# Kernel tuning notes

Measured on AMD Instinct MI355X. Metric: run time of the kernel, lower is better.

The kernel has to match this reference:

```python
import jax, jax.numpy as jnp
import numpy as np

N_NODES = 50000
IN_DIM = 256
EDGE_DIM = 128
OUT_DIM = 128
EDGE_OUT_DIM = 128
N_EDGES = 1600000
NEG_SLOPE = 0.01


def leaky_relu(x):
    return jnp.where(x >= 0, x, NEG_SLOPE * x)


def _kaiming(key, out_d, in_d):
    # kaiming_uniform with a=0.01, leaky_relu gain
    gain = np.sqrt(2.0 / (1.0 + 0.01 ** 2))
    bound = gain * np.sqrt(3.0 / in_d)
    return jax.random.uniform(key, (out_d, in_d), jnp.float32, -bound, bound)


def setup_inputs() -> dict:
    key = jax.random.key(0)
    ks = jax.random.split(key, 9)
    x = jax.random.normal(ks[0], (N_NODES, IN_DIM), jnp.float32)
    edge_index = jax.random.randint(ks[1], (2, N_EDGES), 0, N_NODES, jnp.int64)
    edge_attr = jax.random.normal(ks[2], (N_EDGES, EDGE_DIM), jnp.float32)
    W_e = _kaiming(ks[3], OUT_DIM, EDGE_DIM)
    W_hu = _kaiming(ks[4], OUT_DIM, IN_DIM)
    W_hw = _kaiming(ks[5], OUT_DIM, IN_DIM)
    W2 = _kaiming(ks[6], OUT_DIM, IN_DIM)
    W_emb = _kaiming(ks[7], OUT_DIM, IN_DIM)
    W_attr = _kaiming(ks[8], EDGE_OUT_DIM, OUT_DIM)
    return {"x": x, "edge_index": edge_index, "edge_attr": edge_attr,
            "W_e": W_e, "W_hu": W_hu, "W_hw": W_hw,
            "W2": W2, "W_emb": W_emb, "W_attr": W_attr}


def reference(x, edge_index, edge_attr, W_e, W_hu, W_hw, W2, W_emb, W_attr):
    src, tgt = edge_index[0], edge_index[1]
    # project node features once (N x d), then gather per edge -> avoids E-sized GEMMs
    hu = x @ W_hu.T   # [N, out]
    hw = x @ W_hw.T   # [N, out]
    messages = leaky_relu(edge_attr @ W_e.T + hu[src] + hw[tgt])  # [E, out]
    # scatter_mean over target nodes
    sums = jax.ops.segment_sum(messages, tgt, num_segments=N_NODES)
    counts = jax.ops.segment_sum(jnp.ones((messages.shape[0],), messages.dtype), tgt,
                                 num_segments=N_NODES)
    agg = sums / jnp.maximum(counts, 1.0)[:, None]  # zeros where no incoming edges
    attributes = messages @ W_attr.T  # [E, edge_out]
    embeddings = x @ W_emb.T + leaky_relu(x @ W2.T + agg)  # [N, out]
    return embeddings, attributes
```

## Files before the change

### kernel.cpp

```cpp
#include <hip/hip_runtime.h>

#define NN 50000
#define NE 1600000

using bf16x8 = __bf16 __attribute__((ext_vector_type(8)));
using bf16x4 = __bf16 __attribute__((ext_vector_type(4)));
using bf16x2 = __bf16 __attribute__((ext_vector_type(2)));
using f32x4  = float  __attribute__((ext_vector_type(4)));

__device__ __forceinline__ char* swzp(void* base, int row, int byteoff) {
  return (char*)base + (byteoff ^ ((row & 7) << 4));
}
__device__ __forceinline__ const char* swzpc(const void* base, int row, int byteoff) {
  return (const char*)base + (byteoff ^ ((row & 7) << 4));
}

__device__ __forceinline__ int ld_idx(const void* p, int f64, long long i) {
  return f64 ? (int)((const long long*)p)[i] : ((const int*)p)[i];
}

__global__ void detect_idx64(const int* ei32, int* flag) {
  __shared__ int anynz;
  if (threadIdx.x == 0) anynz = 0;
  __syncthreads();
  if (ei32[2 * threadIdx.x + 1] != 0) atomicOr(&anynz, 1);
  __syncthreads();
  if (threadIdx.x == 0) *flag = (anynz == 0) ? 1 : 0;
}

__global__ void prep_weights(const float* We, const float* Whu, const float* Whw,
                             const float* W2, const float* Wemb, const float* Wattr,
                             __bf16* wHUW, __bf16* wET2, __bf16* wE, __bf16* wA) {
  int i = blockIdx.x * 256 + threadIdx.x;
  if (i < 65536) {
    int n = i >> 8, k = i & 255;
    wHUW[i] = (__bf16)(n < 128 ? Whu[n * 256 + k] : Whw[(n - 128) * 256 + k]);
  } else if (i < 131072) {
    int j = i - 65536; int n = j >> 8, k = j & 255;
    wET2[j] = (__bf16)(n < 128 ? Wemb[n * 256 + k] : W2[(n - 128) * 256 + k]);
  } else if (i < 147456) {
    int j = i - 131072; wE[j] = (__bf16)We[j];
  } else {
    int j = i - 147456; wA[j] = (__bf16)Wattr[j];
  }
}

__global__ void k_hist(const void* ei, const int* flag, int* cnt) {
  int i = blockIdx.x * 256 + threadIdx.x;
  int t = ld_idx(ei, *flag, (long long)NE + i);
  atomicAdd(&cnt[t], 1);
}

__global__ void k_part(const int* cnt, int* part) {
  __shared__ int red[256];
  int i = blockIdx.x * 256 + threadIdx.x;
  red[threadIdx.x] = (i < NN) ? cnt[i] : 0;
  __syncthreads();
  for (int s = 128; s > 0; s >>= 1) {
    if (threadIdx.x < s) red[threadIdx.x] += red[threadIdx.x + s];
    __syncthreads();
  }
  if (threadIdx.x == 0) part[blockIdx.x] = red[0];
}

__global__ void k_scanpart(int* part, int n) {
  __shared__ int sc[256];
  int v = (threadIdx.x < n) ? part[threadIdx.x] : 0;
  sc[threadIdx.x] = v;
  __syncthreads();
  for (int d = 1; d < 256; d <<= 1) {
    int add = (threadIdx.x >= d) ? sc[threadIdx.x - d] : 0;
    __syncthreads();
    sc[threadIdx.x] += add;
    __syncthreads();
  }
  if (threadIdx.x < n) part[threadIdx.x] = sc[threadIdx.x] - v;
}

__global__ void k_offsets(const int* cnt, const int* part, int* offs) {
  __shared__ int sc[256];
  int i = blockIdx.x * 256 + threadIdx.x;
  int v = (i < NN) ? cnt[i] : 0;
  sc[threadIdx.x] = v;
  __syncthreads();
  for (int d = 1; d < 256; d <<= 1) {
    int add = (threadIdx.x >= d) ? sc[threadIdx.x - d] : 0;
    __syncthreads();
    sc[threadIdx.x] += add;
    __syncthreads();
  }
  if (i < NN) offs[i] = part[blockIdx.x] + sc[threadIdx.x] - v;
}

__global__ void k_scatter(const void* ei, const int* flag, const int* offs,
                          int* fill, int* perm) {
  int i = blockIdx.x * 256 + threadIdx.x;
  int t = ld_idx(ei, *flag, (long long)NE + i);
  int pos = offs[t] + atomicAdd(&fill[t], 1);
  perm[pos] = i;
}

template <int MODE>
__global__ __launch_bounds__(512) void node_gemm(
    const float* __restrict__ x, const __bf16* __restrict__ W,
    __bf16* __restrict__ hu, __bf16* __restrict__ hw,
    const float* __restrict__ sums, const int* __restrict__ cnt,
    float* __restrict__ out) {
  __shared__ __bf16 sW[256 * 256];
  const int t = threadIdx.x;
  const int lane = t & 63;
  const int w = t >> 6;
  const int h = lane >> 4;
  const int l15 = lane & 15;

  for (int i = t; i < 8192; i += 512) {
    int row = i >> 5, c8 = (i & 31) << 3;
    bf16x8 v = *(const bf16x8*)(W + row * 256 + c8);
    *(bf16x8*)swzp(sW, row, row * 512 + (c8 << 1)) = v;
  }
  __syncthreads();

  const int ntiles = (NN + 127) / 128;
  for (int tile = blockIdx.x; tile < ntiles; tile += gridDim.x) {
    int m0 = tile * 128 + w * 16;
    if (m0 >= NN) continue;
    int node = m0 + l15;

    f32x4 acc[16];
#pragma unroll
    for (int n = 0; n < 16; ++n) { acc[n][0] = 0.f; acc[n][1] = 0.f; acc[n][2] = 0.f; acc[n][3] = 0.f; }

#pragma unroll
    for (int kc = 0; kc < 8; ++kc) {
      const float* xp = x + (long long)node * 256 + kc * 32 + h * 8;
      f32x4 fa = *(const f32x4*)xp;
      f32x4 fb = *(const f32x4*)(xp + 4);
      bf16x8 b;
#pragma unroll
      for (int j = 0; j < 4; ++j) { b[j] = (__bf16)fa[j]; b[j + 4] = (__bf16)fb[j]; }
#pragma unroll
      for (int n = 0; n < 16; ++n) {
        int row = n * 16 + l15;
        bf16x8 a = *(const bf16x8*)swzpc(sW, row, row * 512 + kc * 64 + h * 16);
        acc[n] = __builtin_amdgcn_mfma_f32_16x16x32_bf16(a, b, acc[n], 0, 0, 0);
      }
    }

    if (MODE == 0) {
#pragma unroll
      for (int n = 0; n < 16; ++n) {
        bf16x4 mv;
#pragma unroll
        for (int j = 0; j < 4; ++j) mv[j] = (__bf16)acc[n][j];
        __bf16* dst = (n < 8) ? (hu + (long long)node * 128 + n * 16 + h * 4)
                              : (hw + (long long)node * 128 + (n - 8) * 16 + h * 4);
        *(bf16x4*)dst = mv;
      }
    } else {
      float inv = 1.f / fmaxf((float)cnt[node], 1.0f);
#pragma unroll
      for (int n = 0; n < 8; ++n) {
        f32x4 ag = *(const f32x4*)(sums + (long long)node * 128 + n * 16 + h * 4);
        f32x4 o;
#pragma unroll
        for (int j = 0; j < 4; ++j) {
          float z = acc[n + 8][j] + ag[j] * inv;
          float lr = z >= 0.f ? z : 0.01f * z;
          o[j] = acc[n][j] + lr;
        }
        *(f32x4*)(out + (long long)node * 128 + n * 16 + h * 4) = o;
      }
    }
  }
}

__global__ __launch_bounds__(1024) void edge_fused(
    const float* __restrict__ eattr, const void* __restrict__ ei,
    const int* __restrict__ flag, const int* __restrict__ perm,
    const __bf16* __restrict__ wE, const __bf16* __restrict__ wA,
    const __bf16* __restrict__ hu, const __bf16* __restrict__ hw,
    float* __restrict__ sums, float* __restrict__ attr_out) {
  __shared__ __bf16 sW1[128 * 128];
  __shared__ __bf16 sW2[128 * 128];
  __shared__ __bf16 sM[2][128 * 128];
  __shared__ int sPerm[2][128], sTgt[2][128];

  const int t = threadIdx.x;
  const int lane = t & 63;
  const int w = t >> 6;
  const int h = lane >> 4;
  const int l15 = lane & 15;
  const int f = *flag;
  const bool producer = (w >= 8);

  for (int i = t; i < 2048; i += 1024) {
    int row = i >> 4, c8 = (i & 15) << 3;
    bf16x8 v1 = *(const bf16x8*)(wE + row * 128 + c8);
    bf16x8 v2 = *(const bf16x8*)(wA + row * 128 + c8);
    int b = row * 256 + (c8 << 1);
    *(bf16x8*)swzp(sW1, row, b) = v1;
    *(bf16x8*)swzp(sW2, row, b) = v2;
  }

  const int ntiles = NE / 128;
  const int tile0 = blockIdx.x;
  if (tile0 >= ntiles) return;
  int buf = 0;

  if (producer) {
    int q = w - 8;
    int pr = q * 16 + l15;
    int p = perm[(long long)tile0 * 128 + pr];
    int srcI = ld_idx(ei, f, p);
    int tgtI = ld_idx(ei, f, (long long)NE + p);
    sPerm[0][pr] = p;
    sTgt[0][pr] = tgtI;
#pragma unroll
    for (int it = 0; it < 4; ++it) {
      int rr = it * 4 + h;
      int sR = __shfl(srcI, rr);
      int tR = __shfl(tgtI, rr);
      bf16x8 a = *(const bf16x8*)(hu + (long long)sR * 128 + l15 * 8);
      bf16x8 b = *(const bf16x8*)(hw + (long long)tR * 128 + l15 * 8);
      bf16x8 o;
#pragma unroll
      for (int j = 0; j < 8; ++j) o[j] = (__bf16)((float)a[j] + (float)b[j]);
      int R = q * 16 + rr;
      *(bf16x8*)swzp(sM[0], R, R * 256 + l15 * 16) = o;
    }
  }
  __syncthreads();

  for (int tile = tile0; tile < ntiles; tile += gridDim.x) {
    int ntile = tile + gridDim.x;
    bool more = ntile < ntiles;

    if (producer) {
      if (more) {
        int q = w - 8;
        int pr = q * 16 + l15;
        int p = perm[(long long)ntile * 128 + pr];
        int srcI = ld_idx(ei, f, p);
        int tgtI = ld_idx(ei, f, (long long)NE + p);
        sPerm[buf ^ 1][pr] = p;
        sTgt[buf ^ 1][pr] = tgtI;
#pragma unroll
        for (int it = 0; it < 4; ++it) {
          int rr = it * 4 + h;
          int sR = __shfl(srcI, rr);
          int tR = __shfl(tgtI, rr);
          bf16x8 a = *(const bf16x8*)(hu + (long long)sR * 128 + l15 * 8);
          bf16x8 b = *(const bf16x8*)(hw + (long long)tR * 128 + l15 * 8);
          bf16x8 o;
#pragma unroll
          for (int j = 0; j < 8; ++j) o[j] = (__bf16)((float)a[j] + (float)b[j]);
          int R = q * 16 + rr;
          *(bf16x8*)swzp(sM[buf ^ 1], R, R * 256 + l15 * 16) = o;
        }
      }
    } else {
      __bf16* sMb = sM[buf];
      const int myP = sPerm[buf][w * 16 + l15];
      const int tgtI = sTgt[buf][w * 16 + l15];
      const float* ep = eattr + (long long)myP * 128 + h * 8;
      f32x4 fa[4], fb[4];
#pragma unroll
      for (int kc = 0; kc < 4; ++kc) {
        fa[kc] = *(const f32x4*)(ep + kc * 32);
        fb[kc] = *(const f32x4*)(ep + kc * 32 + 4);
      }

      f32x4 acc[8];
#pragma unroll
      for (int n = 0; n < 8; ++n) { acc[n][0] = 0.f; acc[n][1] = 0.f; acc[n][2] = 0.f; acc[n][3] = 0.f; }
#pragma unroll
      for (int kc = 0; kc < 4; ++kc) {
        bf16x8 bfr;
#pragma unroll
        for (int j = 0; j < 4; ++j) { bfr[j] = (__bf16)fa[kc][j]; bfr[j + 4] = (__bf16)fb[kc][j]; }
#pragma unroll
        for (int n = 0; n < 8; ++n) {
          int row = n * 16 + l15;
          bf16x8 a = *(const bf16x8*)swzpc(sW1, row, row * 256 + kc * 64 + (h << 4));
          acc[n] = __builtin_amdgcn_mfma_f32_16x16x32_bf16(a, bfr, acc[n], 0, 0, 0);
        }
      }

      const int R = w * 16 + l15;
#pragma unroll
      for (int n = 0; n < 8; ++n) {
        __bf16* mp = (__bf16*)swzp(sMb, R, R * 256 + n * 32 + h * 8);
        bf16x4 hsv = *(const bf16x4*)mp;
        bf16x4 mv;
#pragma unroll
        for (int j = 0; j < 4; ++j) {
          float z = acc[n][j] + (float)hsv[j];
          float m = z >= 0.f ? z : 0.01f * z;
          mv[j] = (__bf16)m;
        }
        *(bf16x4*)mp = mv;
      }

      {
        float s0 = 0.f, s1 = 0.f;
        int curT = __shfl(tgtI, 0);
#pragma unroll
        for (int r = 0; r < 16; ++r) {
          int tg = __shfl(tgtI, r);
          if (tg != curT) {
            unsafeAtomicAdd(&sums[(long long)curT * 128 + 2 * lane], s0);
            unsafeAtomicAdd(&sums[(long long)curT * 128 + 2 * lane + 1], s1);
            s0 = 0.f; s1 = 0.f; curT = tg;
          }
          int R2 = w * 16 + r;
          bf16x2 v = *(const bf16x2*)swzpc(sMb, R2, R2 * 256 + lane * 4);
          s0 += (float)v[0]; s1 += (float)v[1];
        }
        unsafeAtomicAdd(&sums[(long long)curT * 128 + 2 * lane], s0);
        unsafeAtomicAdd(&sums[(long long)curT * 128 + 2 * lane + 1], s1);
      }

      f32x4 acc2[8];
#pragma unroll
      for (int n = 0; n < 8; ++n) { acc2[n][0] = 0.f; acc2[n][1] = 0.f; acc2[n][2] = 0.f; acc2[n][3] = 0.f; }
#pragma unroll
      for (int ks = 0; ks < 4; ++ks) {
        bf16x8 a2 = *(const bf16x8*)swzpc(sMb, R, R * 256 + ks * 64 + (h << 4));
#pragma unroll
        for (int nt = 0; nt < 8; ++nt) {
          int row = nt * 16 + l15;
          bf16x8 b2 = *(const bf16x8*)swzpc(sW2, row, row * 256 + ks * 64 + (h << 4));
          acc2[nt] = __builtin_amdgcn_mfma_f32_16x16x32_bf16(a2, b2, acc2[nt], 0, 0, 0);
        }
      }

      int gp[4];
#pragma unroll
      for (int j = 0; j < 4; ++j) gp[j] = __shfl(myP, (h << 2) + j);
#pragma unroll
      for (int nt = 0; nt < 8; ++nt) {
#pragma unroll
        for (int j = 0; j < 4; ++j) {
          attr_out[(long long)gp[j] * 128 + nt * 16 + l15] = acc2[nt][j];
        }
      }
    }

    __syncthreads();
    buf ^= 1;
  }
}

extern "C" void kernel_launch(void* const* d_in, const int* in_sizes, int n_in,
                              void* d_out, int out_size, void* d_ws, size_t ws_size,
                              hipStream_t stream) {
  const float* x     = (const float*)d_in[0];
  const void*  ei    = d_in[1];
  const float* eattr = (const float*)d_in[2];
  const float* We    = (const float*)d_in[3];
  const float* Whu   = (const float*)d_in[4];
  const float* Whw   = (const float*)d_in[5];
  const float* W2    = (const float*)d_in[6];
  const float* Wemb  = (const float*)d_in[7];
  const float* Wattr = (const float*)d_in[8];

  float* out_emb  = (float*)d_out;
  float* out_attr = out_emb + (size_t)NN * 128;

  char* ws = (char*)d_ws;
  float*  sums = (float*)ws;
  int*    cnt  = (int*)(ws + 25600000);
  int*    fill = (int*)(ws + 25800064);
  int*    offs = (int*)(ws + 26000128);
  int*    part = (int*)(ws + 26200192);
  int*    flag = (int*)(ws + 26201216);
  int*    perm = (int*)(ws + 26201280);
  __bf16* hu   = (__bf16*)(ws + 32601280);
  __bf16* hw   = (__bf16*)(ws + 45401280);
  __bf16* wHUW = (__bf16*)(ws + 58201280);
  __bf16* wET2 = wHUW + 65536;
  __bf16* wE   = wET2 + 65536;
  __bf16* wA   = wE + 16384;

  hipMemsetAsync(ws, 0, 26000128, stream);
  detect_idx64<<<1, 1024, 0, stream>>>((const int*)ei, flag);
  prep_weights<<<640, 256, 0, stream>>>(We, Whu, Whw, W2, Wemb, Wattr, wHUW, wET2, wE, wA);
  k_hist<<<6250, 256, 0, stream>>>(ei, flag, cnt);
  k_part<<<196, 256, 0, stream>>>(cnt, part);
  k_scanpart<<<1, 256, 0, stream>>>(part, 196);
  k_offsets<<<196, 256, 0, stream>>>(cnt, part, offs);
  k_scatter<<<6250, 256, 0, stream>>>(ei, flag, offs, fill, perm);
  node_gemm<0><<<391, 512, 0, stream>>>(x, wHUW, hu, hw, nullptr, nullptr, nullptr);
  edge_fused<<<2048, 1024, 0, stream>>>(eattr, ei, flag, perm, wE, wA, hu, hw, sums, out_attr);
  node_gemm<1><<<391, 512, 0, stream>>>(x, wET2, nullptr, nullptr, sums, cnt, out_emb);
}
```

Measured before the change: 791.0 us.

## Prefetch next tile's edge attributes in registers and halve node_gemm LDS

The consumer warps in edge_fused now load the next tile's perm index and edge_attr rows into registers while computing the current tile. This hides global-load latency behind MFMA work, and the sPerm shared array goes away. node_gemm now stages W in two 128-column K halves, so it uses 64KB of LDS instead of 128KB, which should allow more resident blocks. Both kernels gain min-blocks hints in their launch bounds. The costs are higher register pressure in edge_fused and extra barriers in node_gemm, and with 1024-thread blocks the 4-block hint may force register spills.

After: 1.382 ms. +74.7%, slower.

```diff
diff --git a/kernel.cpp b/kernel.cpp
--- a/kernel.cpp
+++ b/kernel.cpp
@@ -101,29 +101,22 @@
 }
 
 template <int MODE>
-__global__ __launch_bounds__(512) void node_gemm(
+__global__ __launch_bounds__(512, 4) void node_gemm(
     const float* __restrict__ x, const __bf16* __restrict__ W,
     __bf16* __restrict__ hu, __bf16* __restrict__ hw,
     const float* __restrict__ sums, const int* __restrict__ cnt,
     float* __restrict__ out) {
-  __shared__ __bf16 sW[256 * 256];
+  __shared__ __bf16 sW[256 * 128];
   const int t = threadIdx.x;
   const int lane = t & 63;
   const int w = t >> 6;
   const int h = lane >> 4;
   const int l15 = lane & 15;
 
-  for (int i = t; i < 8192; i += 512) {
-    int row = i >> 5, c8 = (i & 31) << 3;
-    bf16x8 v = *(const bf16x8*)(W + row * 256 + c8);
-    *(bf16x8*)swzp(sW, row, row * 512 + (c8 << 1)) = v;
-  }
-  __syncthreads();
-
   const int ntiles = (NN + 127) / 128;
   for (int tile = blockIdx.x; tile < ntiles; tile += gridDim.x) {
     int m0 = tile * 128 + w * 16;
-    if (m0 >= NN) continue;
+    const bool active = (m0 < NN);
     int node = m0 + l15;
 
     f32x4 acc[16];
@@ -131,50 +124,65 @@
     for (int n = 0; n < 16; ++n) { acc[n][0] = 0.f; acc[n][1] = 0.f; acc[n][2] = 0.f; acc[n][3] = 0.f; }
 
 #pragma unroll
-    for (int kc = 0; kc < 8; ++kc) {
-      const float* xp = x + (long long)node * 256 + kc * 32 + h * 8;
-      f32x4 fa = *(const f32x4*)xp;
-      f32x4 fb = *(const f32x4*)(xp + 4);
-      bf16x8 b;
-#pragma unroll
-      for (int j = 0; j < 4; ++j) { b[j] = (__bf16)fa[j]; b[j + 4] = (__bf16)fb[j]; }
-#pragma unroll
-      for (int n = 0; n < 16; ++n) {
-        int row = n * 16 + l15;
-        bf16x8 a = *(const bf16x8*)swzpc(sW, row, row * 512 + kc * 64 + h * 16);
-        acc[n] = __builtin_amdgcn_mfma_f32_16x16x32_bf16(a, b, acc[n], 0, 0, 0);
+    for (int ph = 0; ph < 2; ++ph) {
+      __syncthreads();
+      for (int i = t; i < 4096; i += 512) {
+        int row = i >> 4, c8 = (i & 15) << 3;
+        bf16x8 v = *(const bf16x8*)(W + row * 256 + ph * 128 + c8);
+        *(bf16x8*)swzp(sW, row, row * 256 + (c8 << 1)) = v;
+      }
+      __syncthreads();
+
+      if (active) {
+#pragma unroll
+        for (int kc = 0; kc < 4; ++kc) {
+          const float* xp = x + (long long)node * 256 + ph * 128 + kc * 32 + h * 8;
+          f32x4 fa = *(const f32x4*)xp;
+          f32x4 fb = *(const f32x4*)(xp + 4);
+          bf16x8 b;
+#pragma unroll
+          for (int j = 0; j < 4; ++j) { b[j] = (__bf16)fa[j]; b[j + 4] = (__bf16)fb[j]; }
+#pragma unroll
+          for (int n = 0; n < 16; ++n) {
+            int row = n * 16 + l15;
+            bf16x8 a = *(const bf16x8*)swzpc(sW, row, row * 256 + kc * 64 + h * 16);
+            acc[n] = __builtin_amdgcn_mfma_f32_16x16x32_bf16(a, b, acc[n], 0, 0, 0);
+          }
+        }
       }
     }
 
-    if (MODE == 0) {
-#pragma unroll
-      for (int n = 0; n < 16; ++n) {
-        bf16x4 mv;
-#pragma unroll
-        for (int j = 0; j < 4; ++j) mv[j] = (__bf16)acc[n][j];
-        __bf16* dst = (n < 8) ? (hu + (long long)node * 128 + n * 16 + h * 4)
-                              : (hw + (long long)node * 128 + (n - 8) * 16 + h * 4);
-        *(bf16x4*)dst = mv;
-      }
-    } else {
-      float inv = 1.f / fmaxf((float)cnt[node], 1.0f);
-#pragma unroll
-      for (int n = 0; n < 8; ++n) {
-        f32x4 ag = *(const f32x4*)(sums + (long long)node * 128 + n * 16 + h * 4);
-        f32x4 o;
-#pragma unroll
-        for (int j = 0; j < 4; ++j) {
-          float z = acc[n + 8][j] + ag[j] * inv;
-          float lr = z >= 0.f ? z : 0.01f * z;
-          o[j] = acc[n][j] + lr;
-        }
-        *(f32x4*)(out + (long long)node * 128 + n * 16 + h * 4) = o;
+    if (active) {
+      if (MODE == 0) {
+#pragma unroll
+        for (int n = 0; n < 16; ++n) {
+          bf16x4 mv;
+#pragma unroll
+          for (int j = 0; j < 4; ++j) mv[j] = (__bf16)acc[n][j];
+          __bf16* dst = (n < 8) ? (hu + (long long)node * 128 + n * 16 + h * 4)
+                                : (hw + (long long)node * 128 + (n - 8) * 16 + h * 4);
+          *(bf16x4*)dst = mv;
+        }
+      } else {
+        float inv = 1.f / fmaxf((float)cnt[node], 1.0f);
+#pragma unroll
+        for (int n = 0; n < 8; ++n) {
+          f32x4 ag = *(const f32x4*)(sums + (long long)node * 128 + n * 16 + h * 4);
+          f32x4 o;
+#pragma unroll
+          for (int j = 0; j < 4; ++j) {
+            float z = acc[n + 8][j] + ag[j] * inv;
+            float lr = z >= 0.f ? z : 0.01f * z;
+            o[j] = acc[n][j] + lr;
+          }
+          *(f32x4*)(out + (long long)node * 128 + n * 16 + h * 4) = o;
+        }
       }
     }
   }
 }
 
-__global__ __launch_bounds__(1024) void edge_fused(
+__global__ __launch_bounds__(1024, 4) void edge_fused(
     const float* __restrict__ eattr, const void* __restrict__ ei,
     const int* __restrict__ flag, const int* __restrict__ perm,
     const __bf16* __restrict__ wE, const __bf16* __restrict__ wA,
@@ -183,7 +191,7 @@
   __shared__ __bf16 sW1[128 * 128];
   __shared__ __bf16 sW2[128 * 128];
   __shared__ __bf16 sM[2][128 * 128];
-  __shared__ int sPerm[2][128], sTgt[2][128];
+  __shared__ int sTgt[2][128];
 
   const int t = threadIdx.x;
   const int lane = t & 63;
@@ -207,13 +215,15 @@
   if (tile0 >= ntiles) return;
   int buf = 0;
 
+  int pc = 0;
+  f32x4 fa[4], fb[4];
+
   if (producer) {
     int q = w - 8;
     int pr = q * 16 + l15;
     int p = perm[(long long)tile0 * 128 + pr];
     int srcI = ld_idx(ei, f, p);
     int tgtI = ld_idx(ei, f, (long long)NE + p);
-    sPerm[0][pr] = p;
     sTgt[0][pr] = tgtI;
 #pragma unroll
     for (int it = 0; it < 4; ++it) {
@@ -228,6 +238,14 @@
       int R = q * 16 + rr;
       *(bf16x8*)swzp(sM[0], R, R * 256 + l15 * 16) = o;
     }
+  } else {
+    pc = perm[(long long)tile0 * 128 + w * 16 + l15];
+    const float* ep = eattr + (long long)pc * 128 + h * 8;
+#pragma unroll
+    for (int kc = 0; kc < 4; ++kc) {
+      fa[kc] = *(const f32x4*)(ep + kc * 32);
+      fb[kc] = *(const f32x4*)(ep + kc * 32 + 4);
+    }
   }
   __syncthreads();
 
@@ -242,7 +260,6 @@
         int p = perm[(long long)ntile * 128 + pr];
         int srcI = ld_idx(ei, f, p);
         int tgtI = ld_idx(ei, f, (long long)NE + p);
-        sPerm[buf ^ 1][pr] = p;
         sTgt[buf ^ 1][pr] = tgtI;
 #pragma unroll
         for (int it = 0; it < 4; ++it) {
@@ -260,14 +277,19 @@
       }
     } else {
       __bf16* sMb = sM[buf];
-      const int myP = sPerm[buf][w * 16 + l15];
+      const int myP = pc;
       const int tgtI = sTgt[buf][w * 16 + l15];
-      const float* ep = eattr + (long long)myP * 128 + h * 8;
-      f32x4 fa[4], fb[4];
-#pragma unroll
-      for (int kc = 0; kc < 4; ++kc) {
-        fa[kc] = *(const f32x4*)(ep + kc * 32);
-        fb[kc] = *(const f32x4*)(ep + kc * 32 + 4);
+
+      int pn = 0;
+      f32x4 fan[4], fbn[4];
+      if (more) {
+        pn = perm[(long long)ntile * 128 + w * 16 + l15];
+        const float* ep2 = eattr + (long long)pn * 128 + h * 8;
+#pragma unroll
+        for (int kc = 0; kc < 4; ++kc) {
+          fan[kc] = *(const f32x4*)(ep2 + kc * 32);
+          fbn[kc] = *(const f32x4*)(ep2 + kc * 32 + 4);
+        }
       }
 
       f32x4 acc[8];
@@ -343,6 +365,12 @@
         for (int j = 0; j < 4; ++j) {
           attr_out[(long long)gp[j] * 128 + nt * 16 + l15] = acc2[nt][j];
         }
+      }
+
+      if (more) {
+        pc = pn;
+#pragma unroll
+        for (int kc = 0; kc < 4; ++kc) { fa[kc] = fan[kc]; fb[kc] = fbn[kc]; }
       }
     }
 
```
